# Kernel optimization log

Measured on AMD Instinct MI355X. Metric: run time of the kernel, lower is better.

## Reference

```python
import jax, jax.numpy as jnp
import numpy as np

N_NODES = 40000
N_EDGES = 640000
IN_FEATS = 128
HID = 64
# layer widths per GCN.__init__: in->h->2h->2h->h->h->h->1
DIMS = [IN_FEATS, HID, 2 * HID, 2 * HID, HID, HID, HID, 1]


def setup_inputs() -> dict:
    key = jax.random.key(0)
    ks = jax.random.split(key, 3 + 2 * 7)
    inp = {
        "in_feat": jax.random.normal(ks[0], (N_NODES, IN_FEATS), dtype=jnp.float32),
        "src": jax.random.randint(ks[1], (N_EDGES,), 0, N_NODES, dtype=jnp.int32),
        "dst": jax.random.randint(ks[2], (N_EDGES,), 0, N_NODES, dtype=jnp.int32),
    }
    # DGL GraphConv params: weight [in, out] (glorot), bias [out] (zeros; use small randn for a nontrivial baseline)
    for i in range(7):
        din, dout = DIMS[i], DIMS[i + 1]
        scale = jnp.sqrt(6.0 / (din + dout)).astype(jnp.float32)
        inp[f"W{i+1}"] = jax.random.uniform(ks[3 + 2 * i], (din, dout), jnp.float32, -scale, scale)
        inp[f"b{i+1}"] = 0.01 * jax.random.normal(ks[4 + 2 * i], (dout,), dtype=jnp.float32)
    return inp


def _graph_conv(x, W, b, src, dst, out_norm, in_norm, n_nodes):
    # DGL GraphConv, norm='both', allow_zero_in_degree=True:
    #   h = D_in^{-1/2} * A^T * (D_out^{-1/2} * x) @ W + b
    x = x * out_norm[:, None]
    if x.shape[1] > W.shape[1]:
        # mult W first to shrink message dim (mirrors DGL's heuristic; math-equivalent)
        x = x @ W
        h = jax.ops.segment_sum(x[src], dst, num_segments=n_nodes)
    else:
        h = jax.ops.segment_sum(x[src], dst, num_segments=n_nodes)
        h = h @ W
    return h * in_norm[:, None] + b


def reference(in_feat, src, dst, W1, b1, W2, b2, W3, b3, W4, b4, W5, b5, W6, b6, W7, b7):
    n = in_feat.shape[0]
    ones = jnp.ones((src.shape[0],), dtype=jnp.float32)
    out_deg = jax.ops.segment_sum(ones, src, num_segments=n)
    in_deg = jax.ops.segment_sum(ones, dst, num_segments=n)
    out_norm = jnp.where(out_deg > 0, jax.lax.rsqrt(jnp.maximum(out_deg, 1.0)), 0.0)
    in_norm = jnp.where(in_deg > 0, jax.lax.rsqrt(jnp.maximum(in_deg, 1.0)), 0.0)

    params = [(W1, b1), (W2, b2), (W3, b3), (W4, b4), (W5, b5), (W6, b6), (W7, b7)]
    h = in_feat
    for i, (W, b) in enumerate(params):
        h = _graph_conv(h, W, b, src, dst, out_norm, in_norm, n)
        if i < 6:
            h = jax.nn.relu(h)
    return h  # [N, 1]
```

## Files before the change

### kernel.cpp

```cpp
#include <hip/hip_runtime.h>
#include <hip/hip_bf16.h>


#define IN_F 128
#define NSLICE 60
#define SHB 13
#define NSHARD 5

typedef __attribute__((ext_vector_type(8))) short short8v;
typedef __attribute__((ext_vector_type(4))) float f32x4;
typedef __attribute__((ext_vector_type(8))) _Float16 half8v;

static __device__ __forceinline__ unsigned short f2bf(float x) {
    unsigned u = __builtin_bit_cast(unsigned, x);
    unsigned r = (u + 0x7FFFu + ((u >> 16) & 1u)) >> 16;
    return (unsigned short)r;
}
static __device__ __forceinline__ float bf2f(unsigned short h) {
    unsigned u = ((unsigned)h) << 16;
    return __builtin_bit_cast(float, u);
}


__global__ __launch_bounds__(256) void hist2_kernel(const int* __restrict__ src,
                                                    const int* __restrict__ dst,
                                                    int* __restrict__ scratch, int E) {
    constexpr int SH = 1 << SHB;
    __shared__ int h[SH];
    const int t = threadIdx.x;
    const int b = blockIdx.x;
    const int s = blockIdx.y;
    const int z = blockIdx.z;
    const int* idx = z ? dst : src;
    for (int i = t; i < SH; i += 256) h[i] = 0;
    __syncthreads();
    const int per = (E + NSLICE - 1) / NSLICE;
    const int lo = b * per;
    const int hiE = min(lo + per, E);
    const int base = s << SHB;
    for (int e = lo + t; e < hiE; e += 256) {
        unsigned a = (unsigned)(idx[e] - base);
        if (a < (unsigned)SH) atomicAdd(&h[a], 1);
    }
    __syncthreads();
    int* so = scratch + ((size_t)((z * NSHARD + s) * NSLICE + b) << SHB);
    for (int i = t; i < SH; i += 256) so[i] = h[i];
}

__global__ void hist_reduce_kernel(const int* __restrict__ scratch,
                                   int* __restrict__ in_deg,
                                   float* __restrict__ out_nrm,
                                   float* __restrict__ in_nrm, int N) {
    constexpr int SH = 1 << SHB;
    int n = blockIdx.x * blockDim.x + threadIdx.x;
    if (n >= N) return;
    int s = n >> SHB;
    int i = n & (SH - 1);
    int od = 0, idg = 0;
    for (int b = 0; b < NSLICE; ++b) {
        od  += scratch[((size_t)((0 * NSHARD + s) * NSLICE + b) << SHB) + i];
        idg += scratch[((size_t)((1 * NSHARD + s) * NSLICE + b) << SHB) + i];
    }
    in_deg[n] = idg;
    out_nrm[n] = od  > 0 ? rsqrtf((float)od)  : 0.f;
    in_nrm[n]  = idg > 0 ? rsqrtf((float)idg) : 0.f;
}


__global__ __launch_bounds__(256) void scan_blk_kernel(const int* __restrict__ deg,
                                                       int* __restrict__ blockSums, int N) {
    __shared__ int ws[4];
    const int t = threadIdx.x;
    const int base = blockIdx.x * 1024 + t * 4;
    int4 v = make_int4(0, 0, 0, 0);
    if (base + 3 < N) v = *reinterpret_cast<const int4*>(&deg[base]);
    else if (base < N) {
        v.x = deg[base];
        if (base + 1 < N) v.y = deg[base + 1];
        if (base + 2 < N) v.z = deg[base + 2];
    }
    int s = v.x + v.y + v.z + v.w;
#pragma unroll
    for (int off = 32; off > 0; off >>= 1) s += __shfl_down(s, off);
    if ((t & 63) == 0) ws[t >> 6] = s;
    __syncthreads();
    if (t == 0) blockSums[blockIdx.x] = ws[0] + ws[1] + ws[2] + ws[3];
}

__global__ __launch_bounds__(64) void scan_top_kernel(const int* __restrict__ blockSums,
                                                      int* __restrict__ blockOffs,
                                                      int* __restrict__ row_off, int NB, int N) {
    const int t = threadIdx.x;
    int orig = (t < NB) ? blockSums[t] : 0;
    int v = orig;
#pragma unroll
    for (int off = 1; off < 64; off <<= 1) {
        int u = __shfl_up(v, off);
        if (t >= off) v += u;
    }
    if (t < NB) blockOffs[t] = v - orig;
    if (t == 63) row_off[N] = v;
}

__global__ __launch_bounds__(256) void scan_fill_kernel(const int* __restrict__ deg,
                                                        const int* __restrict__ blockOffs,
                                                        int* __restrict__ row_off, int N) {
    __shared__ int wtot[4];
    const int t = threadIdx.x;
    const int lane = t & 63;
    const int wid = t >> 6;
    const int base = blockIdx.x * 1024 + t * 4;
    int4 v = make_int4(0, 0, 0, 0);
    if (base + 3 < N) v = *reinterpret_cast<const int4*>(&deg[base]);
    else if (base < N) {
        v.x = deg[base];
        if (base + 1 < N) v.y = deg[base + 1];
        if (base + 2 < N) v.z = deg[base + 2];
    }
    const int s = v.x + v.y + v.z + v.w;
    int incl = s;
#pragma unroll
    for (int off = 1; off < 64; off <<= 1) {
        int u = __shfl_up(incl, off);
        if (lane >= off) incl += u;
    }
    if (lane == 63) wtot[wid] = incl;
    __syncthreads();
    int pre = blockOffs[blockIdx.x] + incl - s;
    for (int i = 0; i < wid; ++i) pre += wtot[i];
    if (base < N) {
        int run = pre;
        row_off[base] = run; run += v.x;
        if (base + 1 < N) { row_off[base + 1] = run; run += v.y; }
        if (base + 2 < N) { row_off[base + 2] = run; run += v.z; }
        if (base + 3 < N) { row_off[base + 3] = run; }
    }
}

__global__ void slice_base_kernel(int* __restrict__ scratch,
                                  const int* __restrict__ row_off, int N) {
    constexpr int SH = 1 << SHB;
    int n = blockIdx.x * blockDim.x + threadIdx.x;
    if (n >= N) return;
    int s = n >> SHB;
    int i = n & (SH - 1);
    int run = row_off[n];
    for (int b = 0; b < NSLICE; ++b) {
        size_t off = ((size_t)((NSHARD + s) * NSLICE + b) << SHB) + i;
        int c = scratch[off];
        scratch[off] = run;
        run += c;
    }
}

__global__ __launch_bounds__(256) void fill2_kernel(const int* __restrict__ src,
                                                    const int* __restrict__ dst,
                                                    const int* __restrict__ scratch,
                                                    int* __restrict__ csr, int E) {
    constexpr int SH = 1 << SHB;
    __shared__ int cur[SH];
    const int t = threadIdx.x;
    const int b = blockIdx.x;
    const int s = blockIdx.y;
    const int* base = scratch + ((size_t)((NSHARD + s) * NSLICE + b) << SHB);
    for (int i = t; i < SH; i += 256) cur[i] = base[i];
    __syncthreads();
    const int per = (E + NSLICE - 1) / NSLICE;
    const int lo = b * per;
    const int hiE = min(lo + per, E);
    const int nb = s << SHB;
    for (int e = lo + t; e < hiE; e += 256) {
        unsigned a = (unsigned)(dst[e] - nb);
        if (a < (unsigned)SH) {
            int pos = atomicAdd(&cur[a], 1);
            csr[pos] = src[e];
        }
    }
}


struct WDesc { const float* w; unsigned short* th; unsigned short* tl; int K; int N; };
struct WPack { WDesc d[6]; };

__global__ __launch_bounds__(256) void split_w_kernel(WPack p) {
    WDesc d = p.d[blockIdx.x];
    int i = blockIdx.y * 256 + threadIdx.x;
    if (i >= d.K * d.N) return;
    int k = i / d.N, n = i - k * d.N;
    float v = d.w[i];
    unsigned short h = f2bf(v);
    d.th[(size_t)n * d.K + k] = h;
    d.tl[(size_t)n * d.K + k] = f2bf(v - bf2f(h));
}


template<int K, int NOUT>
__global__ __launch_bounds__(256) void gemm_mfma_f32(
    const float* __restrict__ X,
    const unsigned short* __restrict__ Bh, const unsigned short* __restrict__ Bl,
    const float* __restrict__ pre, _Float16* __restrict__ Y16, int M) {
    constexpr int NT = NOUT / 16;
    const int lane = threadIdx.x & 63;
    const int wv = threadIdx.x >> 6;
    const int r0 = blockIdx.x * 64 + wv * 16;
    const int arow = r0 + (lane & 15);
    const int kg = (lane >> 4) * 8;
    const float sc = pre[arow];

    f32x4 acc[NT];
#pragma unroll
    for (int n = 0; n < NT; ++n) acc[n] = (f32x4){0.f, 0.f, 0.f, 0.f};

    for (int kk = 0; kk < K; kk += 32) {
        const float* ap = &X[(size_t)arow * K + kk + kg];
        float4 v0 = *reinterpret_cast<const float4*>(ap);
        float4 v1 = *reinterpret_cast<const float4*>(ap + 4);
        float a[8] = {v0.x, v0.y, v0.z, v0.w, v1.x, v1.y, v1.z, v1.w};
        short8v a_h, a_l;
#pragma unroll
        for (int j = 0; j < 8; ++j) {
            float f = a[j] * sc;
            unsigned short hh = f2bf(f);
            a_h[j] = (short)hh;
            a_l[j] = (short)f2bf(f - bf2f(hh));
        }
#pragma unroll
        for (int n = 0; n < NT; ++n) {
            int col = n * 16 + (lane & 15);
            short8v b_h = *reinterpret_cast<const short8v*>(Bh + (size_t)col * K + kk + kg);
            short8v b_l = *reinterpret_cast<const short8v*>(Bl + (size_t)col * K + kk + kg);
            acc[n] = __builtin_amdgcn_mfma_f32_16x16x32_bf16(a_h, b_h, acc[n], 0, 0, 0);
            acc[n] = __builtin_amdgcn_mfma_f32_16x16x32_bf16(a_h, b_l, acc[n], 0, 0, 0);
            acc[n] = __builtin_amdgcn_mfma_f32_16x16x32_bf16(a_l, b_h, acc[n], 0, 0, 0);
        }
    }
    const int c0 = lane & 15;
    const int rr = r0 + (lane >> 4) * 4;
#pragma unroll
    for (int n = 0; n < NT; ++n) {
        const int col = n * 16 + c0;
#pragma unroll
        for (int j = 0; j < 4; ++j)
            Y16[(size_t)(rr + j) * NOUT + col] = (_Float16)acc[n][j];
    }
}


template<int K, int NOUT>
__global__ __launch_bounds__(256) void gemm_mfma(
    const unsigned short* __restrict__ Ah, const unsigned short* __restrict__ Al,
    const unsigned short* __restrict__ Bh, const unsigned short* __restrict__ Bl,
    _Float16* __restrict__ Y16, int M) {
    constexpr int NT = NOUT / 16;
    const int lane = threadIdx.x & 63;
    const int wv = threadIdx.x >> 6;
    const int r0 = blockIdx.x * 64 + wv * 16;
    const int arow = r0 + (lane & 15);
    const int kg = (lane >> 4) * 8;

    f32x4 acc[NT];
#pragma unroll
    for (int n = 0; n < NT; ++n) acc[n] = (f32x4){0.f, 0.f, 0.f, 0.f};

    for (int kk = 0; kk < K; kk += 32) {
        short8v a_h = *reinterpret_cast<const short8v*>(Ah + (size_t)arow * K + kk + kg);
        short8v a_l = *reinterpret_cast<const short8v*>(Al + (size_t)arow * K + kk + kg);
#pragma unroll
        for (int n = 0; n < NT; ++n) {
            int col = n * 16 + (lane & 15);
            short8v b_h = *reinterpret_cast<const short8v*>(Bh + (size_t)col * K + kk + kg);
            short8v b_l = *reinterpret_cast<const short8v*>(Bl + (size_t)col * K + kk + kg);
            acc[n] = __builtin_amdgcn_mfma_f32_16x16x32_bf16(a_h, b_h, acc[n], 0, 0, 0);
            acc[n] = __builtin_amdgcn_mfma_f32_16x16x32_bf16(a_h, b_l, acc[n], 0, 0, 0);
            acc[n] = __builtin_amdgcn_mfma_f32_16x16x32_bf16(a_l, b_h, acc[n], 0, 0, 0);
        }
    }
    const int c0 = lane & 15;
    const int rr = r0 + (lane >> 4) * 4;
#pragma unroll
    for (int n = 0; n < NT; ++n) {
        const int col = n * 16 + c0;
#pragma unroll
        for (int j = 0; j < 4; ++j)
            Y16[(size_t)(rr + j) * NOUT + col] = (_Float16)acc[n][j];
    }
}


template<int K, int NOUT, int OUTM>
__global__ __launch_bounds__(256) void fused_ag(
    const _Float16* __restrict__ X, const int* __restrict__ csr,
    const int* __restrict__ row_off,
    const unsigned short* __restrict__ Bh, const unsigned short* __restrict__ Bl,
    const float* __restrict__ r_nrm, const float* __restrict__ s_nrm,
    const float* __restrict__ bias,
    _Float16* __restrict__ Y16, unsigned short* __restrict__ Yh,
    unsigned short* __restrict__ Yl, int N) {
    constexpr int G = K / 8;
    constexpr int LPE = G;
    constexpr int EPW = 64 / LPE;
    constexpr int NT = NOUT / 16;
    __shared__ unsigned short sAh[64 * K];
    __shared__ unsigned short sAl[64 * K];
    const int lane = threadIdx.x & 63;
    const int wv = threadIdx.x >> 6;
    const int g = lane / LPE;
    const int c = lane % LPE;
    const int nodeBase = blockIdx.x * 64 + wv * 16;

    for (int i = 0; i < 16; ++i) {
        const int node = nodeBase + i;
        if (node >= N) break;
        const int lo = row_off[node];
        const int hi = row_off[node + 1];
        float acc[8], acc2[8];
#pragma unroll
        for (int j = 0; j < 8; ++j) { acc[j] = 0.f; acc2[j] = 0.f; }
        int e = lo + g;
        for (; e + EPW < hi; e += 2 * EPW) {
            int s0 = csr[e];
            int s1 = csr[e + EPW];
            half8v x0 = *reinterpret_cast<const half8v*>(&X[(size_t)s0 * K + c * 8]);
            half8v x1 = *reinterpret_cast<const half8v*>(&X[(size_t)s1 * K + c * 8]);
#pragma unroll
            for (int j = 0; j < 8; ++j) { acc[j] += (float)x0[j]; acc2[j] += (float)x1[j]; }
        }
        if (e < hi) {
            int s0 = csr[e];
            half8v x0 = *reinterpret_cast<const half8v*>(&X[(size_t)s0 * K + c * 8]);
#pragma unroll
            for (int j = 0; j < 8; ++j) acc[j] += (float)x0[j];
        }
#pragma unroll
        for (int j = 0; j < 8; ++j) acc[j] += acc2[j];
#pragma unroll
        for (int m = LPE; m < 64; m <<= 1) {
#pragma unroll
            for (int j = 0; j < 8; ++j) acc[j] += __shfl_xor(acc[j], m);
        }
        if (lane < LPE) {
            const int row = wv * 16 + i;
            short8v hv, lv;
#pragma unroll
            for (int j = 0; j < 8; ++j) {
                unsigned short hh = f2bf(acc[j]);
                hv[j] = (short)hh;
                lv[j] = (short)f2bf(acc[j] - bf2f(hh));
            }
            const int grp = c ^ (row & (G - 1));
            *reinterpret_cast<short8v*>(&sAh[row * K + grp * 8]) = hv;
            *reinterpret_cast<short8v*>(&sAl[row * K + grp * 8]) = lv;
        }
    }
    __syncthreads();

    const int arow = wv * 16 + (lane & 15);
    f32x4 oacc[NT];
#pragma unroll
    for (int n = 0; n < NT; ++n) oacc[n] = (f32x4){0.f, 0.f, 0.f, 0.f};

    for (int kk = 0; kk < K; kk += 32) {
        const int gidx = (kk >> 3) + (lane >> 4);
        const int grp = gidx ^ (arow & (G - 1));
        short8v a_h = *reinterpret_cast<const short8v*>(&sAh[arow * K + grp * 8]);
        short8v a_l = *reinterpret_cast<const short8v*>(&sAl[arow * K + grp * 8]);
        const int kg = (lane >> 4) * 8;
#pragma unroll
        for (int n = 0; n < NT; ++n) {
            int col = n * 16 + (lane & 15);
            short8v b_h = *reinterpret_cast<const short8v*>(Bh + (size_t)col * K + kk + kg);
            short8v b_l = *reinterpret_cast<const short8v*>(Bl + (size_t)col * K + kk + kg);
            oacc[n] = __builtin_amdgcn_mfma_f32_16x16x32_bf16(a_h, b_h, oacc[n], 0, 0, 0);
            oacc[n] = __builtin_amdgcn_mfma_f32_16x16x32_bf16(a_h, b_l, oacc[n], 0, 0, 0);
            oacc[n] = __builtin_amdgcn_mfma_f32_16x16x32_bf16(a_l, b_h, oacc[n], 0, 0, 0);
        }
    }

    const int c0 = lane & 15;
    const int rr = blockIdx.x * 64 + wv * 16 + (lane >> 4) * 4;
#pragma unroll
    for (int n = 0; n < NT; ++n) {
        const int col = n * 16 + c0;
        const float bcol = bias[col];
#pragma unroll
        for (int j = 0; j < 4; ++j) {
            const int row = rr + j;
            float y = fmaf(oacc[n][j], r_nrm[row], bcol);
            y = fmaxf(y, 0.f);
            y *= s_nrm[row];
            if (OUTM == 0) {
                Y16[(size_t)row * NOUT + col] = (_Float16)y;
            } else {
                unsigned short h = f2bf(y);
                Yh[(size_t)row * NOUT + col] = h;
                Yl[(size_t)row * NOUT + col] = f2bf(y - bf2f(h));
            }
        }
    }
}


template<int F>
__global__ __launch_bounds__(256) void agg_h16(
    const _Float16* __restrict__ X, const int* __restrict__ csr,
    const int* __restrict__ row_off, const float* __restrict__ r_nrm,
    const float* __restrict__ s_nrm, const float* __restrict__ bias,
    _Float16* __restrict__ Y16, int N) {
    constexpr int LPE = F / 8;
    constexpr int EPW = 64 / LPE;
    const int lane = threadIdx.x & 63;
    const int node = blockIdx.x * (blockDim.x >> 6) + (threadIdx.x >> 6);
    if (node >= N) return;
    const int g = lane / LPE;
    const int c = lane % LPE;
    const int lo = row_off[node];
    const int hi = row_off[node + 1];
    float acc[8], acc2[8];
#pragma unroll
    for (int j = 0; j < 8; ++j) { acc[j] = 0.f; acc2[j] = 0.f; }
    int e = lo + g;
    for (; e + EPW < hi; e += 2 * EPW) {
        int s0 = csr[e];
        int s1 = csr[e + EPW];
        half8v x0 = *reinterpret_cast<const half8v*>(&X[(size_t)s0 * F + c * 8]);
        half8v x1 = *reinterpret_cast<const half8v*>(&X[(size_t)s1 * F + c * 8]);
#pragma unroll
        for (int j = 0; j < 8; ++j) { acc[j] += (float)x0[j]; acc2[j] += (float)x1[j]; }
    }
    if (e < hi) {
        int s0 = csr[e];
        half8v x0 = *reinterpret_cast<const half8v*>(&X[(size_t)s0 * F + c * 8]);
#pragma unroll
        for (int j = 0; j < 8; ++j) acc[j] += (float)x0[j];
    }
#pragma unroll
    for (int j = 0; j < 8; ++j) acc[j] += acc2[j];
#pragma unroll
    for (int m = LPE; m < 64; m <<= 1) {
#pragma unroll
        for (int j = 0; j < 8; ++j) acc[j] += __shfl_xor(acc[j], m);
    }
    if (lane < LPE) {
        float rn = r_nrm[node];
        float sn = s_nrm[node];
        half8v o;
#pragma unroll
        for (int j = 0; j < 8; ++j) {
            float y = fmaf(acc[j], rn, bias[lane * 8 + j]);
            y = fmaxf(y, 0.f) * sn;
            o[j] = (_Float16)y;
        }
        *reinterpret_cast<half8v*>(&Y16[(size_t)node * F + lane * 8]) = o;
    }
}


__global__ __launch_bounds__(256) void gemv64_kernel(const _Float16* __restrict__ X,
                                                     const float* __restrict__ W,
                                                     float* __restrict__ Y, int M) {
    const int lane = threadIdx.x & 63;
    const int m = blockIdx.x * (blockDim.x >> 6) + (threadIdx.x >> 6);
    if (m >= M) return;
    float v = (float)X[(size_t)m * 64 + lane] * W[lane];
#pragma unroll
    for (int off = 32; off > 0; off >>= 1) v += __shfl_down(v, off);
    if (lane == 0) Y[m] = v;
}

__global__ __launch_bounds__(256) void agg1_kernel(const float* __restrict__ T,
                                                   const int* __restrict__ csr,
                                                   const int* __restrict__ row_off,
                                                   const float* __restrict__ r_nrm,
                                                   const float* __restrict__ bias,
                                                   float* __restrict__ Y, int N) {
    const int node = blockIdx.x * 16 + (threadIdx.x >> 4);
    const int l = threadIdx.x & 15;
    if (node >= N) return;
    const int lo = row_off[node];
    const int hi = row_off[node + 1];
    float acc = 0.f;
    for (int e = lo + l; e < hi; e += 16) acc += T[csr[e]];
#pragma unroll
    for (int m = 8; m >= 1; m >>= 1) acc += __shfl_xor(acc, m);
    if (l == 0) Y[node] = fmaf(acc, r_nrm[node], bias[0]);
}


extern "C" void kernel_launch(void* const* d_in, const int* in_sizes, int n_in,
                              void* d_out, int out_size, void* d_ws, size_t ws_size,
                              hipStream_t stream) {
    const float* in_feat = (const float*)d_in[0];
    const int* src = (const int*)d_in[1];
    const int* dst = (const int*)d_in[2];
    const float* W1 = (const float*)d_in[3];  const float* B1 = (const float*)d_in[4];
    const float* W2 = (const float*)d_in[5];  const float* B2 = (const float*)d_in[6];
    const float* W3 = (const float*)d_in[7];  const float* B3 = (const float*)d_in[8];
    const float* W4 = (const float*)d_in[9];  const float* B4 = (const float*)d_in[10];
    const float* W5 = (const float*)d_in[11]; const float* B5 = (const float*)d_in[12];
    const float* W6 = (const float*)d_in[13]; const float* B6 = (const float*)d_in[14];
    const float* W7 = (const float*)d_in[15]; const float* B7 = (const float*)d_in[16];

    const int N = in_sizes[0] / IN_F;
    const int E = in_sizes[1];
    float* out = (float*)d_out;

    char* w = (char*)d_ws;
    auto alloc = [&](size_t bytes) { char* p = w; w += (bytes + 255) & ~(size_t)255; return p; };
    int* csr      = (int*)alloc((size_t)E * 4);
    int* row_off  = (int*)alloc((size_t)(N + 1) * 4);
    int* in_deg   = (int*)alloc((size_t)N * 4);
    int* blockSums= (int*)alloc(64 * 4);
    int* blockOffs= (int*)alloc(64 * 4);
    float* out_nrm= (float*)alloc((size_t)N * 4);
    float* in_nrm = (float*)alloc((size_t)N * 4);
    float* t7     = (float*)alloc((size_t)N * 4);
    const int dims[8] = {128, 64, 128, 128, 64, 64, 64, 1};
    unsigned short* wth[6]; unsigned short* wtl[6];
    for (int i = 0; i < 6; ++i) {
        size_t kn = (size_t)dims[i] * dims[i + 1];
        wth[i] = (unsigned short*)alloc(kn * 2);
        wtl[i] = (unsigned short*)alloc(kn * 2);
    }
    unsigned short* th = (unsigned short*)alloc((size_t)N * 128 * 2);
    unsigned short* tl = (unsigned short*)alloc((size_t)N * 128 * 2);
    _Float16* h0 = (_Float16*)alloc((size_t)N * 128 * 2);
    _Float16* h1 = (_Float16*)alloc((size_t)N * 128 * 2);
    int* scratch = (int*)th;
    (void)ws_size; (void)n_in; (void)out_size;

    const int TB = 256;
    const int NB = (N + 1023) / 1024;

    WPack wp;
    const float* Ws[6] = {W1, W2, W3, W4, W5, W6};
    for (int i = 0; i < 6; ++i) wp.d[i] = {Ws[i], wth[i], wtl[i], dims[i], dims[i + 1]};
    split_w_kernel<<<dim3(6, 64), TB, 0, stream>>>(wp);

    hist2_kernel<<<dim3(NSLICE, NSHARD, 2), TB, 0, stream>>>(src, dst, scratch, E);
    hist_reduce_kernel<<<(N + TB - 1) / TB, TB, 0, stream>>>(
        scratch, in_deg, out_nrm, in_nrm, N);
    scan_blk_kernel<<<NB, TB, 0, stream>>>(in_deg, blockSums, N);
    scan_top_kernel<<<1, 64, 0, stream>>>(blockSums, blockOffs, row_off, NB, N);
    scan_fill_kernel<<<NB, TB, 0, stream>>>(in_deg, blockOffs, row_off, N);
    slice_base_kernel<<<(N + TB - 1) / TB, TB, 0, stream>>>(scratch, row_off, N);
    fill2_kernel<<<dim3(NSLICE, NSHARD), TB, 0, stream>>>(src, dst, scratch, csr, E);

    const int gridN4 = (N + 3) / 4;
    const int MB = (N + 63) / 64;

    gemm_mfma_f32<128, 64><<<MB, TB, 0, stream>>>(in_feat, wth[0], wtl[0], out_nrm, h0, N);
    agg_h16<64><<<gridN4, TB, 0, stream>>>(h0, csr, row_off, in_nrm, out_nrm, B1, h1, N);

    fused_ag<64, 128, 0><<<MB, TB, 0, stream>>>(
        h1, csr, row_off, wth[1], wtl[1], in_nrm, out_nrm, B2, h0, nullptr, nullptr, N);

    fused_ag<128, 128, 1><<<MB, TB, 0, stream>>>(
        h0, csr, row_off, wth[2], wtl[2], in_nrm, out_nrm, B3, nullptr, th, tl, N);

    gemm_mfma<128, 64><<<MB, TB, 0, stream>>>(th, tl, wth[3], wtl[3], h1, N);
    agg_h16<64><<<gridN4, TB, 0, stream>>>(h1, csr, row_off, in_nrm, out_nrm, B4, h0, N);

    fused_ag<64, 64, 0><<<MB, TB, 0, stream>>>(
        h0, csr, row_off, wth[4], wtl[4], in_nrm, out_nrm, B5, h1, nullptr, nullptr, N);

    fused_ag<64, 64, 0><<<MB, TB, 0, stream>>>(
        h1, csr, row_off, wth[5], wtl[5], in_nrm, out_nrm, B6, h0, nullptr, nullptr, N);

    gemv64_kernel<<<gridN4, TB, 0, stream>>>(h0, W7, t7, N);
    agg1_kernel<<<(N + 15) / 16, TB, 0, stream>>>(t7, csr, row_off, in_nrm, B7, out, N);
}
```

Baseline: 347.9 us.

## Unfuse aggregation from GEMM into separate high-parallelism gather and fp16-input GEMM kernels

Replaces the fused aggregate-then-GEMM kernels with a plain per-node aggregation kernel (one wave per node) followed by a GEMM that reads fp16 activations and splits them into bf16 hi/lo pairs in registers. The intent is to stop each wave serially gathering 16 nodes with large LDS footprint, which limited occupancy and latency hiding. It also drops the separate bf16 hi/lo intermediate buffers in favour of fp16 storage. The trade is extra kernel launches, an extra global round trip of intermediates, and slightly lower precision for the layer-3 output.

```diff
diff --git a/kernel.cpp b/kernel.cpp
--- a/kernel.cpp
+++ b/kernel.cpp
@@ -246,11 +246,12 @@
 }
 
 
-template<int K, int NOUT>
-__global__ __launch_bounds__(256) void gemm_mfma(
-    const unsigned short* __restrict__ Ah, const unsigned short* __restrict__ Al,
+template<int K, int NOUT, bool EPI>
+__global__ __launch_bounds__(256) void gemm_h16(
+    const _Float16* __restrict__ X,
     const unsigned short* __restrict__ Bh, const unsigned short* __restrict__ Bl,
-    _Float16* __restrict__ Y16, int M) {
+    const float* __restrict__ r_nrm, const float* __restrict__ s_nrm,
+    const float* __restrict__ bias, _Float16* __restrict__ Y16, int M) {
     constexpr int NT = NOUT / 16;
     const int lane = threadIdx.x & 63;
     const int wv = threadIdx.x >> 6;
@@ -263,8 +264,15 @@
     for (int n = 0; n < NT; ++n) acc[n] = (f32x4){0.f, 0.f, 0.f, 0.f};
 
     for (int kk = 0; kk < K; kk += 32) {
-        short8v a_h = *reinterpret_cast<const short8v*>(Ah + (size_t)arow * K + kk + kg);
-        short8v a_l = *reinterpret_cast<const short8v*>(Al + (size_t)arow * K + kk + kg);
+        half8v av = *reinterpret_cast<const half8v*>(&X[(size_t)arow * K + kk + kg]);
+        short8v a_h, a_l;
+#pragma unroll
+        for (int j = 0; j < 8; ++j) {
+            float f = (float)av[j];
+            unsigned short hh = f2bf(f);
+            a_h[j] = (short)hh;
+            a_l[j] = (short)f2bf(f - bf2f(hh));
+        }
 #pragma unroll
         for (int n = 0; n < NT; ++n) {
             int col = n * 16 + (lane & 15);
@@ -280,127 +288,23 @@
 #pragma unroll
     for (int n = 0; n < NT; ++n) {
         const int col = n * 16 + c0;
-#pragma unroll
-        for (int j = 0; j < 4; ++j)
-            Y16[(size_t)(rr + j) * NOUT + col] = (_Float16)acc[n][j];
-    }
-}
-
-
-template<int K, int NOUT, int OUTM>
-__global__ __launch_bounds__(256) void fused_ag(
-    const _Float16* __restrict__ X, const int* __restrict__ csr,
-    const int* __restrict__ row_off,
-    const unsigned short* __restrict__ Bh, const unsigned short* __restrict__ Bl,
-    const float* __restrict__ r_nrm, const float* __restrict__ s_nrm,
-    const float* __restrict__ bias,
-    _Float16* __restrict__ Y16, unsigned short* __restrict__ Yh,
-    unsigned short* __restrict__ Yl, int N) {
-    constexpr int G = K / 8;
-    constexpr int LPE = G;
-    constexpr int EPW = 64 / LPE;
-    constexpr int NT = NOUT / 16;
-    __shared__ unsigned short sAh[64 * K];
-    __shared__ unsigned short sAl[64 * K];
-    const int lane = threadIdx.x & 63;
-    const int wv = threadIdx.x >> 6;
-    const int g = lane / LPE;
-    const int c = lane % LPE;
-    const int nodeBase = blockIdx.x * 64 + wv * 16;
-
-    for (int i = 0; i < 16; ++i) {
-        const int node = nodeBase + i;
-        if (node >= N) break;
-        const int lo = row_off[node];
-        const int hi = row_off[node + 1];
-        float acc[8], acc2[8];
-#pragma unroll
-        for (int j = 0; j < 8; ++j) { acc[j] = 0.f; acc2[j] = 0.f; }
-        int e = lo + g;
-        for (; e + EPW < hi; e += 2 * EPW) {
-            int s0 = csr[e];
-            int s1 = csr[e + EPW];
-            half8v x0 = *reinterpret_cast<const half8v*>(&X[(size_t)s0 * K + c * 8]);
-            half8v x1 = *reinterpret_cast<const half8v*>(&X[(size_t)s1 * K + c * 8]);
-#pragma unroll
-            for (int j = 0; j < 8; ++j) { acc[j] += (float)x0[j]; acc2[j] += (float)x1[j]; }
-        }
-        if (e < hi) {
-            int s0 = csr[e];
-            half8v x0 = *reinterpret_cast<const half8v*>(&X[(size_t)s0 * K + c * 8]);
-#pragma unroll
-            for (int j = 0; j < 8; ++j) acc[j] += (float)x0[j];
-        }
-#pragma unroll
-        for (int j = 0; j < 8; ++j) acc[j] += acc2[j];
-#pragma unroll
-        for (int m = LPE; m < 64; m <<= 1) {
-#pragma unroll
-            for (int j = 0; j < 8; ++j) acc[j] += __shfl_xor(acc[j], m);
-        }
-        if (lane < LPE) {
-            const int row = wv * 16 + i;
-            short8v hv, lv;
-#pragma unroll
-            for (int j = 0; j < 8; ++j) {
-                unsigned short hh = f2bf(acc[j]);
-                hv[j] = (short)hh;
-                lv[j] = (short)f2bf(acc[j] - bf2f(hh));
-            }
-            const int grp = c ^ (row & (G - 1));
-            *reinterpret_cast<short8v*>(&sAh[row * K + grp * 8]) = hv;
-            *reinterpret_cast<short8v*>(&sAl[row * K + grp * 8]) = lv;
-        }
-    }
-    __syncthreads();
-
-    const int arow = wv * 16 + (lane & 15);
-    f32x4 oacc[NT];
-#pragma unroll
-    for (int n = 0; n < NT; ++n) oacc[n] = (f32x4){0.f, 0.f, 0.f, 0.f};
-
-    for (int kk = 0; kk < K; kk += 32) {
-        const int gidx = (kk >> 3) + (lane >> 4);
-        const int grp = gidx ^ (arow & (G - 1));
-        short8v a_h = *reinterpret_cast<const short8v*>(&sAh[arow * K + grp * 8]);
-        short8v a_l = *reinterpret_cast<const short8v*>(&sAl[arow * K + grp * 8]);
-        const int kg = (lane >> 4) * 8;
-#pragma unroll
-        for (int n = 0; n < NT; ++n) {
-            int col = n * 16 + (lane & 15);
-            short8v b_h = *reinterpret_cast<const short8v*>(Bh + (size_t)col * K + kk + kg);
-            short8v b_l = *reinterpret_cast<const short8v*>(Bl + (size_t)col * K + kk + kg);
-            oacc[n] = __builtin_amdgcn_mfma_f32_16x16x32_bf16(a_h, b_h, oacc[n], 0, 0, 0);
-            oacc[n] = __builtin_amdgcn_mfma_f32_16x16x32_bf16(a_h, b_l, oacc[n], 0, 0, 0);
-            oacc[n] = __builtin_amdgcn_mfma_f32_16x16x32_bf16(a_l, b_h, oacc[n], 0, 0, 0);
-        }
-    }
-
-    const int c0 = lane & 15;
-    const int rr = blockIdx.x * 64 + wv * 16 + (lane >> 4) * 4;
-#pragma unroll
-    for (int n = 0; n < NT; ++n) {
-        const int col = n * 16 + c0;
-        const float bcol = bias[col];
+        const float bcol = EPI ? bias[col] : 0.f;
 #pragma unroll
         for (int j = 0; j < 4; ++j) {
             const int row = rr + j;
-            float y = fmaf(oacc[n][j], r_nrm[row], bcol);
-            y = fmaxf(y, 0.f);
-            y *= s_nrm[row];
-            if (OUTM == 0) {
-                Y16[(size_t)row * NOUT + col] = (_Float16)y;
-            } else {
-                unsigned short h = f2bf(y);
-                Yh[(size_t)row * NOUT + col] = h;
-                Yl[(size_t)row * NOUT + col] = f2bf(y - bf2f(h));
+            float y = acc[n][j];
+            if (EPI) {
+                y = fmaf(y, r_nrm[row], bcol);
+                y = fmaxf(y, 0.f);
+                y *= s_nrm[row];
             }
-        }
-    }
-}
-
-
-template<int F>
+            Y16[(size_t)row * NOUT + col] = (_Float16)y;
+        }
+    }
+}
+
+
+template<int F, bool EPI>
 __global__ __launch_bounds__(256) void agg_h16(
     const _Float16* __restrict__ X, const int* __restrict__ csr,
     const int* __restrict__ row_off, const float* __restrict__ r_nrm,
@@ -441,14 +345,18 @@
         for (int j = 0; j < 8; ++j) acc[j] += __shfl_xor(acc[j], m);
     }
     if (lane < LPE) {
-        float rn = r_nrm[node];
-        float sn = s_nrm[node];
         half8v o;
-#pragma unroll
-        for (int j = 0; j < 8; ++j) {
-            float y = fmaf(acc[j], rn, bias[lane * 8 + j]);
-            y = fmaxf(y, 0.f) * sn;
-            o[j] = (_Float16)y;
+        if (EPI) {
+            float rn = r_nrm[node];
+            float sn = s_nrm[node];
+#pragma unroll
+            for (int j = 0; j < 8; ++j) {
+                float y = fmaf(acc[j], rn, bias[lane * 8 + j]);
+                o[j] = (_Float16)(fmaxf(y, 0.f) * sn);
+            }
+        } else {
+#pragma unroll
+            for (int j = 0; j < 8; ++j) o[j] = (_Float16)acc[j];
         }
         *reinterpret_cast<half8v*>(&Y16[(size_t)node * F + lane * 8]) = o;
     }
@@ -521,11 +429,9 @@
         wth[i] = (unsigned short*)alloc(kn * 2);
         wtl[i] = (unsigned short*)alloc(kn * 2);
     }
-    unsigned short* th = (unsigned short*)alloc((size_t)N * 128 * 2);
-    unsigned short* tl = (unsigned short*)alloc((size_t)N * 128 * 2);
     _Float16* h0 = (_Float16*)alloc((size_t)N * 128 * 2);
     _Float16* h1 = (_Float16*)alloc((size_t)N * 128 * 2);
-    int* scratch = (int*)th;
+    int* scratch = (int*)h0;
     (void)ws_size; (void)n_in; (void)out_size;
 
     const int TB = 256;
@@ -549,23 +455,23 @@
     const int MB = (N + 63) / 64;
 
     gemm_mfma_f32<128, 64><<<MB, TB, 0, stream>>>(in_feat, wth[0], wtl[0], out_nrm, h0, N);
-    agg_h16<64><<<gridN4, TB, 0, stream>>>(h0, csr, row_off, in_nrm, out_nrm, B1, h1, N);
-
-    fused_ag<64, 128, 0><<<MB, TB, 0, stream>>>(
-        h1, csr, row_off, wth[1], wtl[1], in_nrm, out_nrm, B2, h0, nullptr, nullptr, N);
-
-    fused_ag<128, 128, 1><<<MB, TB, 0, stream>>>(
-        h0, csr, row_off, wth[2], wtl[2], in_nrm, out_nrm, B3, nullptr, th, tl, N);
-
-    gemm_mfma<128, 64><<<MB, TB, 0, stream>>>(th, tl, wth[3], wtl[3], h1, N);
-    agg_h16<64><<<gridN4, TB, 0, stream>>>(h1, csr, row_off, in_nrm, out_nrm, B4, h0, N);
-
-    fused_ag<64, 64, 0><<<MB, TB, 0, stream>>>(
-        h0, csr, row_off, wth[4], wtl[4], in_nrm, out_nrm, B5, h1, nullptr, nullptr, N);
-
-    fused_ag<64, 64, 0><<<MB, TB, 0, stream>>>(
-        h1, csr, row_off, wth[5], wtl[5], in_nrm, out_nrm, B6, h0, nullptr, nullptr, N);
-
-    gemv64_kernel<<<gridN4, TB, 0, stream>>>(h0, W7, t7, N);
+    agg_h16<64, true><<<gridN4, TB, 0, stream>>>(h0, csr, row_off, in_nrm, out_nrm, B1, h1, N);
+
+    agg_h16<64, false><<<gridN4, TB, 0, stream>>>(h1, csr, row_off, nullptr, nullptr, nullptr, h0, N);
+    gemm_h16<64, 128, true><<<MB, TB, 0, stream>>>(h0, wth[1], wtl[1], in_nrm, out_nrm, B2, h1, N);
+
+    agg_h16<128, false><<<gridN4, TB, 0, stream>>>(h1, csr, row_off, nullptr, nullptr, nullptr, h0, N);
+    gemm_h16<128, 128, true><<<MB, TB, 0, stream>>>(h0, wth[2], wtl[2], in_nrm, out_nrm, B3, h1, N);
+
+    gemm_h16<128, 64, false><<<MB, TB, 0, stream>>>(h1, wth[3], wtl[3], nullptr, nullptr, nullptr, h0, N);
+    agg_h16<64, true><<<gridN4, TB, 0, stream>>>(h0, csr, row_off, in_nrm, out_nrm, B4, h1, N);
+
+    agg_h16<64, false><<<gridN4, TB, 0, stream>>>(h1, csr, row_off, nullptr, nullptr, nullptr, h0, N);
+    gemm_h16<64, 64, true><<<MB, TB, 0, stream>>>(h0, wth[4], wtl[4], in_nrm, out_nrm, B5, h1, N);
+
+    agg_h16<64, false><<<gridN4, TB, 0, stream>>>(h1, csr, row_off, nullptr, nullptr, nullptr, h0, N);
+    gemm_h16<64, 64, true><<<MB, TB, 0, stream>>>(h0, wth[5], wtl[5], in_nrm, out_nrm, B6, h1, N);
+
+    gemv64_kernel<<<gridN4, TB, 0, stream>>>(h1, W7, t7, N);
     agg1_kernel<<<(N + 15) / 16, TB, 0, stream>>>(t7, csr, row_off, in_nrm, B7, out, N);
 }
```

Result: faster. 306.0 us (-12.0%).
